# Kernel tuning notes

Hardware: AMD Instinct MI355X
Metric: run time of the kernel (lower is better)

## Reference

```python
import jax, jax.numpy as jnp
import numpy as np

N = 50000
E = 800000
IN_DIM = 256
OUT_DIM = 128
HEADS = 4
D_K = OUT_DIM // HEADS  # 32
BETA = 1.0  # beta_init, requires_grad=False (constant)
NEG_SLOPE = 0.2
EPS = 1e-12


def setup_inputs() -> dict:
    key = jax.random.key(0)
    k = jax.random.split(key, 8)
    H = jax.random.normal(k[0], (N, IN_DIM), dtype=jnp.float32)
    edge_index = jax.random.randint(k[1], (2, E), 0, N, dtype=jnp.int64)
    sim1_edge = jax.random.normal(k[2], (E,), dtype=jnp.float32)
    # Parameters (torch nn.Linear stores weight as (out, in); y = x @ W.T)
    W = jax.random.normal(k[3], (HEADS * D_K, IN_DIM), dtype=jnp.float32) * (1.0 / np.sqrt(IN_DIM))
    a_src = jax.random.normal(k[4], (HEADS, D_K), dtype=jnp.float32)
    a_dst = jax.random.normal(k[5], (HEADS, D_K), dtype=jnp.float32)
    msg_lin_w = jax.random.normal(k[6], (D_K, D_K), dtype=jnp.float32) * (1.0 / np.sqrt(D_K))
    return {"H": H, "edge_index": edge_index, "sim1_edge": sim1_edge,
            "W": W, "a_src": a_src, "a_dst": a_dst, "msg_lin_w": msg_lin_w}


def reference(H, edge_index, sim1_edge, W, a_src, a_dst, msg_lin_w):
    n = H.shape[0]
    H_proj = (H @ W.T).reshape(n, HEADS, D_K)           # [N, h, d_k]
    src, dst = edge_index[0], edge_index[1]
    h_src = H_proj[src]                                  # [E, h, d_k]
    h_dst = H_proj[dst]                                  # [E, h, d_k]
    # per-edge attention logits (struct + semantic)
    e = (jnp.einsum('ehd,hd->eh', h_src, a_src)
         + jnp.einsum('ehd,hd->eh', h_dst, a_dst)
         + BETA * sim1_edge[:, None])                    # [E, h]
    e = jnp.where(e >= 0, e, NEG_SLOPE * e)              # LeakyReLU(0.2)
    # global (per-head) max for stabilization, matching original e.max(dim=0)
    e = e - jnp.max(e, axis=0, keepdims=True)
    exp_e = jnp.exp(e)                                   # [E, h]
    denom = jax.ops.segment_sum(exp_e, dst, num_segments=n)  # [N, h]
    alpha = exp_e / (denom[dst] + EPS)                   # [E, h]  (dropout p=0 -> identity)
    m = alpha[:, :, None] * h_src                        # [E, h, d_k]
    out = jax.ops.segment_sum(m, dst, num_segments=n)    # [N, h, d_k]
    out_h = out.reshape(n, HEADS * D_K)                  # concat=True
    msg_base = jnp.einsum('ehd,od->eho', h_src, msg_lin_w).mean(axis=1)  # [E, d_k]
    alpha_mean = alpha.mean(axis=1)                      # [E]
    return out_h, alpha_mean, msg_base
```

## Files before the change

kernel.cpp:

```cpp
#include <hip/hip_runtime.h>
#include <hip/hip_bf16.h>
#include <hip/hip_fp16.h>
#include <float.h>

#define HEADS 4
#define DK 32

static constexpr float kBeta = 1.0f;
static constexpr float kNeg  = 0.2f;
static constexpr float kEps  = 1e-12f;

__device__ __forceinline__ float bf2f(unsigned short v) {
  return __uint_as_float((unsigned)v << 16);
}
__device__ __forceinline__ float2 bfp2(unsigned u) {
  return make_float2(__uint_as_float(u << 16), __uint_as_float(u & 0xFFFF0000u));
}
__device__ __forceinline__ unsigned fkey(float x) {
  unsigned u = __float_as_uint(x);
  return (u & 0x80000000u) ? ~u : (u | 0x80000000u);
}
__device__ __forceinline__ float funkey(unsigned k) {
  unsigned u = (k & 0x80000000u) ? (k & 0x7fffffffu) : ~k;
  return __uint_as_float(u);
}

__global__ __launch_bounds__(256) void k_detect(const int* __restrict__ ei32,
                                                const unsigned* __restrict__ Hw,
                                                int* __restrict__ eflag,
                                                int* __restrict__ dflag,
                                                int E, int nw) {
  int i = blockIdx.x * 256 + threadIdx.x;
  if (i < 4096 && 2 * i + 1 < 2 * E && ei32[2 * i + 1] != 0) atomicOr(eflag, 1);
  if (i < nw && ((Hw[i] >> 7) & 0xFFu) == 0xFFu) atomicOr(dflag, 1);
}

__global__ __launch_bounds__(256) void k_cvt(const int* __restrict__ ei32,
                                             const int* __restrict__ eflag,
                                             int* __restrict__ src_i,
                                             int* __restrict__ dst_i,
                                             int* __restrict__ deg, int E) {
  int i = blockIdx.x * 256 + threadIdx.x;
  if (i >= E) return;
  int s, d;
  if (*eflag) { s = ei32[i];     d = ei32[E + i]; }
  else        { s = ei32[2 * i]; d = ei32[2 * E + 2 * i]; }
  src_i[i] = s;
  dst_i[i] = d;
  atomicAdd(deg + d, 1);
}

__global__ __launch_bounds__(256) void k_params(const void* __restrict__ a_src,
                                                const void* __restrict__ a_dst,
                                                const void* __restrict__ msg_w,
                                                float* __restrict__ af,
                                                float* __restrict__ msgwf,
                                                const int* __restrict__ dflag) {
  int i = blockIdx.x * 256 + threadIdx.x;
  int dt = *dflag;
  if (i < 128) {
    af[i] = dt ? ((const float*)a_src)[i] : bf2f(((const unsigned short*)a_src)[i]);
  } else if (i < 256) {
    int j = i - 128;
    af[i] = dt ? ((const float*)a_dst)[j] : bf2f(((const unsigned short*)a_dst)[j]);
  } else if (i < 1280) {
    int j = i - 256;
    msgwf[j] = dt ? ((const float*)msg_w)[j] : bf2f(((const unsigned short*)msg_w)[j]);
  }
}

__global__ __launch_bounds__(256) void k_wcvt(const void* __restrict__ in,
                                              float* __restrict__ out,
                                              const int* __restrict__ dflag, int n) {
  int i = blockIdx.x * 256 + threadIdx.x;
  if (i >= n) return;
  int r = i >> 8, c = i & 255;
  float v = (*dflag) ? ((const float*)in)[i] : bf2f(((const unsigned short*)in)[i]);
  out[(size_t)c * 128 + r] = v;
}

__global__ __launch_bounds__(256) void k_scan1(const int* __restrict__ deg,
                                               int* __restrict__ bsum, int N) {
  const int t = threadIdx.x;
  int i = blockIdx.x * 256 + t;
  int v = (i < N) ? deg[i] : 0;
#pragma unroll
  for (int off = 32; off; off >>= 1) v += __shfl_xor(v, off);
  __shared__ int red[4];
  if ((t & 63) == 0) red[t >> 6] = v;
  __syncthreads();
  if (t == 0) bsum[blockIdx.x] = red[0] + red[1] + red[2] + red[3];
}
__global__ __launch_bounds__(1024) void k_scan2(int* __restrict__ bsum, int nb) {
  __shared__ int part[1024];
  const int t = threadIdx.x;
  part[t] = (t < nb) ? bsum[t] : 0;
  __syncthreads();
  int own = part[t];
  for (int off = 1; off < 1024; off <<= 1) {
    int v = (t >= off) ? part[t - off] : 0;
    __syncthreads();
    part[t] += v;
    __syncthreads();
  }
  if (t < nb) bsum[t] = part[t] - own;
}
__global__ __launch_bounds__(256) void k_scan3(const int* __restrict__ deg,
                                               const int* __restrict__ bsum,
                                               int* __restrict__ row_ptr,
                                               int* __restrict__ cursor, int N) {
  __shared__ int part[256];
  const int t = threadIdx.x;
  int i = blockIdx.x * 256 + t;
  int v = (i < N) ? deg[i] : 0;
  part[t] = v;
  __syncthreads();
  for (int off = 1; off < 256; off <<= 1) {
    int x = (t >= off) ? part[t - off] : 0;
    __syncthreads();
    part[t] += x;
    __syncthreads();
  }
  int excl = part[t] - v + bsum[blockIdx.x];
  if (i < N) {
    row_ptr[i] = excl;
    cursor[i]  = excl;
    if (i == N - 1) row_ptr[N] = excl + v;
  }
}

__global__ __launch_bounds__(256) void k_fill(const int* __restrict__ dst,
                                              int* __restrict__ cursor,
                                              int* __restrict__ eidx, int E) {
  int e = blockIdx.x * 256 + threadIdx.x;
  if (e >= E) return;
  int pos = atomicAdd(cursor + dst[e], 1);
  eidx[pos] = e;
}

__global__ __launch_bounds__(256) void k_proj(const void* __restrict__ Hraw,
                                              const float* __restrict__ Wtf,
                                              const int* __restrict__ dflag,
                                              float* __restrict__ Hproj, int N) {
  __shared__ float Ht[32][260];
  const int t = threadIdx.x;
  const int nb = blockIdx.x * 32;
  const int dt = *dflag;
  if (dt) {
    const float4* __restrict__ H4 = (const float4*)Hraw;
#pragma unroll
    for (int i = 0; i < 8; ++i) {
      int f = t + i * 256;
      int r = f >> 6, kq = f & 63;
      float4 v = make_float4(0.f, 0.f, 0.f, 0.f);
      if (nb + r < N) v = H4[(size_t)(nb + r) * 64 + kq];
      *(float4*)&Ht[r][4 * kq] = v;
    }
  } else {
    const uint4* __restrict__ H8 = (const uint4*)Hraw;
#pragma unroll
    for (int i = 0; i < 4; ++i) {
      int g = t + i * 256;
      int r = g >> 5, c8 = g & 31;
      uint4 v = make_uint4(0u, 0u, 0u, 0u);
      if (nb + r < N) v = H8[(size_t)(nb + r) * 32 + c8];
      float2 f0 = bfp2(v.x), f1 = bfp2(v.y), f2 = bfp2(v.z), f3 = bfp2(v.w);
      *(float4*)&Ht[r][c8 * 8 + 0] = make_float4(f0.x, f0.y, f1.x, f1.y);
      *(float4*)&Ht[r][c8 * 8 + 4] = make_float4(f2.x, f2.y, f3.x, f3.y);
    }
  }
  __syncthreads();
  const int cg = (t & 31);
  const int n0 = (t >> 5) * 4;
  float acc[4][4];
#pragma unroll
  for (int n = 0; n < 4; ++n)
#pragma unroll
    for (int j = 0; j < 4; ++j) acc[n][j] = 0.f;
  const float4* __restrict__ Wt4 = (const float4*)Wtf;
#pragma unroll 4
  for (int kk = 0; kk < 256; kk += 4) {
    float4 w0 = Wt4[(size_t)(kk + 0) * 32 + cg];
    float4 w1 = Wt4[(size_t)(kk + 1) * 32 + cg];
    float4 w2 = Wt4[(size_t)(kk + 2) * 32 + cg];
    float4 w3 = Wt4[(size_t)(kk + 3) * 32 + cg];
#pragma unroll
    for (int n = 0; n < 4; ++n) {
      float4 h = *(const float4*)&Ht[n0 + n][kk];
      acc[n][0] += h.x * w0.x + h.y * w1.x + h.z * w2.x + h.w * w3.x;
      acc[n][1] += h.x * w0.y + h.y * w1.y + h.z * w2.y + h.w * w3.y;
      acc[n][2] += h.x * w0.z + h.y * w1.z + h.z * w2.z + h.w * w3.z;
      acc[n][3] += h.x * w0.w + h.y * w1.w + h.z * w2.w + h.w * w3.w;
    }
  }
#pragma unroll
  for (int n = 0; n < 4; ++n) {
    int row = nb + n0 + n;
    if (row < N)
      *(float4*)&Hproj[(size_t)row * 128 + 4 * cg] =
          make_float4(acc[n][0], acc[n][1], acc[n][2], acc[n][3]);
  }
}

__global__ __launch_bounds__(256) void k_node(const float* __restrict__ Hproj,
                                              const float* __restrict__ af,
                                              const float* __restrict__ msgwf,
                                              float* __restrict__ s_src,
                                              float* __restrict__ s_dst,
                                              __half* __restrict__ msgb,
                                              __half* __restrict__ Hb, int N) {
  const int l = threadIdx.x & 63;
  const int wb = threadIdx.x >> 6;
  const int n = (blockIdx.x << 2) + wb;
  if (n >= N) return;
  const float* row = Hproj + (size_t)n * 128;
  float h0 = row[l], h1 = row[64 + l];
  Hb[(size_t)n * 128 + l]      = __float2half(h0);
  Hb[(size_t)n * 128 + 64 + l] = __float2half(h1);
  float p0 = h0 * af[l],       p1 = h1 * af[64 + l];
  float q0 = h0 * af[128 + l], q1 = h1 * af[192 + l];
#pragma unroll
  for (int off = 16; off; off >>= 1) {
    p0 += __shfl_xor(p0, off);
    p1 += __shfl_xor(p1, off);
    q0 += __shfl_xor(q0, off);
    q1 += __shfl_xor(q1, off);
  }
  if (l == 0)  { s_src[n*4+0] = p0; s_src[n*4+2] = p1; s_dst[n*4+0] = q0; s_dst[n*4+2] = q1; }
  if (l == 32) { s_src[n*4+1] = p0; s_src[n*4+3] = p1; s_dst[n*4+1] = q0; s_dst[n*4+3] = q1; }
  float t4 = h0 + __shfl_xor(h0, 32) + h1 + __shfl_xor(h1, 32);
  float hbar = 0.25f * t4;
  if (l < DK) {
    float acc = 0.f;
#pragma unroll
    for (int d = 0; d < DK; ++d) acc += __shfl(hbar, d) * msgwf[l * DK + d];
    msgb[(size_t)n * DK + l] = __float2half(acc);
  }
}

__global__ __launch_bounds__(256) void k_logits(const int* __restrict__ src,
                                                const int* __restrict__ dst,
                                                const void* __restrict__ sim1,
                                                const int* __restrict__ dflag,
                                                const float* __restrict__ s_src,
                                                const float* __restrict__ s_dst,
                                                unsigned* __restrict__ gmax, int E) {
  const int e = blockIdx.x * 256 + threadIdx.x;
  float m0 = -FLT_MAX, m1 = -FLT_MAX, m2 = -FLT_MAX, m3 = -FLT_MAX;
  if (e < E) {
    int s = src[e], d = dst[e];
    float4 ss = *(const float4*)(s_src + (size_t)s * 4);
    float4 sd = *(const float4*)(s_dst + (size_t)d * 4);
    float sv = (*dflag) ? ((const float*)sim1)[e] : bf2f(((const unsigned short*)sim1)[e]);
    float b = kBeta * sv;
    float e0 = ss.x + sd.x + b; e0 = (e0 >= 0.f) ? e0 : kNeg * e0;
    float e1 = ss.y + sd.y + b; e1 = (e1 >= 0.f) ? e1 : kNeg * e1;
    float e2 = ss.z + sd.z + b; e2 = (e2 >= 0.f) ? e2 : kNeg * e2;
    float e3 = ss.w + sd.w + b; e3 = (e3 >= 0.f) ? e3 : kNeg * e3;
    m0 = e0; m1 = e1; m2 = e2; m3 = e3;
  }
#pragma unroll
  for (int off = 32; off; off >>= 1) {
    m0 = fmaxf(m0, __shfl_xor(m0, off));
    m1 = fmaxf(m1, __shfl_xor(m1, off));
    m2 = fmaxf(m2, __shfl_xor(m2, off));
    m3 = fmaxf(m3, __shfl_xor(m3, off));
  }
  __shared__ float red[4][4];
  if ((threadIdx.x & 63) == 0) {
    int w = threadIdx.x >> 6;
    red[w][0] = m0; red[w][1] = m1; red[w][2] = m2; red[w][3] = m3;
  }
  __syncthreads();
  if (threadIdx.x < 4) {
    int h = threadIdx.x;
    float mm = fmaxf(fmaxf(red[0][h], red[1][h]), fmaxf(red[2][h], red[3][h]));
    atomicMax(gmax + h, fkey(mm));
  }
}

__global__ __launch_bounds__(256) void k_msg(const int* __restrict__ src,
                                             const __half2* __restrict__ msgb2,
                                             const int* __restrict__ dflag,
                                             void* __restrict__ d_out,
                                             int N, int E) {
  long long tid = (long long)blockIdx.x * 256 + threadIdx.x;
  if (tid >= (long long)E * 16) return;
  int e = (int)(tid >> 4), jp = (int)(tid & 15);
  __half2 hv = msgb2[(size_t)src[e] * 16 + jp];
  float2 f = __half22float2(hv);
  const size_t msg_off = (size_t)N * 128 + (size_t)E;
  if (*dflag) {
    *(float2*)&((float*)d_out)[msg_off + (size_t)e * 32 + 2 * jp] = f;
  } else {
    __hip_bfloat162 b = __float22bfloat162_rn(f);
    *(__hip_bfloat162*)((__hip_bfloat16*)d_out + msg_off + (size_t)e * 32 + 2 * jp) = b;
  }
}

__global__ __launch_bounds__(256) void k_out(const int* __restrict__ row_ptr,
                                             const int* __restrict__ eidx,
                                             const int* __restrict__ src,
                                             const void* __restrict__ sim1,
                                             const float* __restrict__ s_src,
                                             const float* __restrict__ s_dst,
                                             const unsigned* __restrict__ gmax,
                                             const unsigned* __restrict__ Hb_u,
                                             const int* __restrict__ dflag,
                                             void* __restrict__ d_out, int N, int E) {
  const int n = (int)((blockIdx.x * 256 + threadIdx.x) >> 6);
  const int l = threadIdx.x & 63;
  if (n >= N) return;
  const int beg = row_ptr[n];
  const int deg = row_ptr[n + 1] - beg;
  const int dt = *dflag;
  const float m0 = funkey(gmax[0]), m1 = funkey(gmax[1]);
  const float m2 = funkey(gmax[2]), m3 = funkey(gmax[3]);
  const float4 sd = *(const float4*)(s_dst + (size_t)n * 4);
  const size_t alpha_off = (size_t)N * 128;
  float accx = 0.f, accy = 0.f;
  float4 dn = make_float4(0.f, 0.f, 0.f, 0.f);
  int eid = 0, s = 0;
  float4 ev = make_float4(0.f, 0.f, 0.f, 0.f);
  const bool small = (deg <= 64);
  if (small) {
    if (l < deg) {
      eid = eidx[beg + l];
      s = src[eid];
      float4 ss = *(const float4*)(s_src + (size_t)s * 4);
      float sv = dt ? ((const float*)sim1)[eid] : bf2f(((const unsigned short*)sim1)[eid]);
      float e0 = ss.x + sd.x + sv; e0 = (e0 >= 0.f) ? e0 : kNeg * e0;
      float e1 = ss.y + sd.y + sv; e1 = (e1 >= 0.f) ? e1 : kNeg * e1;
      float e2 = ss.z + sd.z + sv; e2 = (e2 >= 0.f) ? e2 : kNeg * e2;
      float e3 = ss.w + sd.w + sv; e3 = (e3 >= 0.f) ? e3 : kNeg * e3;
      ev = make_float4(expf(e0 - m0), expf(e1 - m1), expf(e2 - m2), expf(e3 - m3));
      dn = ev;
    }
  } else {
    for (int base = 0; base < deg; base += 64) {
      if (base + l < deg) {
        int e2i = eidx[beg + base + l];
        int s2 = src[e2i];
        float4 ss = *(const float4*)(s_src + (size_t)s2 * 4);
        float sv = dt ? ((const float*)sim1)[e2i] : bf2f(((const unsigned short*)sim1)[e2i]);
        float e0 = ss.x + sd.x + sv; e0 = (e0 >= 0.f) ? e0 : kNeg * e0;
        float e1 = ss.y + sd.y + sv; e1 = (e1 >= 0.f) ? e1 : kNeg * e1;
        float e2 = ss.z + sd.z + sv; e2 = (e2 >= 0.f) ? e2 : kNeg * e2;
        float e3 = ss.w + sd.w + sv; e3 = (e3 >= 0.f) ? e3 : kNeg * e3;
        dn.x += expf(e0 - m0); dn.y += expf(e1 - m1);
        dn.z += expf(e2 - m2); dn.w += expf(e3 - m3);
      }
    }
  }
#pragma unroll
  for (int off = 32; off; off >>= 1) {
    dn.x += __shfl_xor(dn.x, off);
    dn.y += __shfl_xor(dn.y, off);
    dn.z += __shfl_xor(dn.z, off);
    dn.w += __shfl_xor(dn.w, off);
  }
  const float i0 = 1.f / (dn.x + kEps), i1 = 1.f / (dn.y + kEps);
  const float i2 = 1.f / (dn.z + kEps), i3 = 1.f / (dn.w + kEps);
  const float myinv = (l < 32) ? ((l < 16) ? i0 : i1) : ((l < 48) ? i2 : i3);
  if (small) {
    if (l < deg) {
      float am = 0.25f * (ev.x * i0 + ev.y * i1 + ev.z * i2 + ev.w * i3);
      if (dt) ((float*)d_out)[alpha_off + eid] = am;
      else    ((__hip_bfloat16*)d_out)[alpha_off + eid] = __float2bfloat16(am);
    }
    for (int i = 0; i < deg; ++i) {
      int si = __shfl(s, i);
      float ax = __shfl(ev.x, i), ay = __shfl(ev.y, i);
      float az = __shfl(ev.z, i), aw = __shfl(ev.w, i);
      float aa = ((l < 32) ? ((l < 16) ? ax : ay) : ((l < 48) ? az : aw)) * myinv;
      unsigned u = Hb_u[(size_t)si * 64 + l];
      float2 f = __half22float2(*(const __half2*)&u);
      accx += aa * f.x;
      accy += aa * f.y;
    }
  } else {
    for (int base = 0; base < deg; base += 64) {
      int cnt = min(64, deg - base);
      int eid2 = 0, s2 = 0;
      float4 e2v = make_float4(0.f, 0.f, 0.f, 0.f);
      if (l < cnt) {
        eid2 = eidx[beg + base + l];
        s2 = src[eid2];
        float4 ss = *(const float4*)(s_src + (size_t)s2 * 4);
        float sv = dt ? ((const float*)sim1)[eid2] : bf2f(((const unsigned short*)sim1)[eid2]);
        float e0 = ss.x + sd.x + sv; e0 = (e0 >= 0.f) ? e0 : kNeg * e0;
        float e1 = ss.y + sd.y + sv; e1 = (e1 >= 0.f) ? e1 : kNeg * e1;
        float e2 = ss.z + sd.z + sv; e2 = (e2 >= 0.f) ? e2 : kNeg * e2;
        float e3 = ss.w + sd.w + sv; e3 = (e3 >= 0.f) ? e3 : kNeg * e3;
        e2v = make_float4(expf(e0 - m0), expf(e1 - m1), expf(e2 - m2), expf(e3 - m3));
        float am = 0.25f * (e2v.x * i0 + e2v.y * i1 + e2v.z * i2 + e2v.w * i3);
        if (dt) ((float*)d_out)[alpha_off + eid2] = am;
        else    ((__hip_bfloat16*)d_out)[alpha_off + eid2] = __float2bfloat16(am);
      }
      for (int i = 0; i < cnt; ++i) {
        int si = __shfl(s2, i);
        float ax = __shfl(e2v.x, i), ay = __shfl(e2v.y, i);
        float az = __shfl(e2v.z, i), aw = __shfl(e2v.w, i);
        float aa = ((l < 32) ? ((l < 16) ? ax : ay) : ((l < 48) ? az : aw)) * myinv;
        unsigned u = Hb_u[(size_t)si * 64 + l];
        float2 f = __half22float2(*(const __half2*)&u);
        accx += aa * f.x;
        accy += aa * f.y;
      }
    }
  }
  if (dt) {
    *(float2*)&((float*)d_out)[(size_t)n * 128 + 2 * l] = make_float2(accx, accy);
  } else {
    __hip_bfloat162 b = __float22bfloat162_rn(make_float2(accx, accy));
    *(__hip_bfloat162*)((__hip_bfloat16*)d_out + (size_t)n * 128 + 2 * l) = b;
  }
}

extern "C" void kernel_launch(void* const* d_in, const int* in_sizes, int n_in,
                              void* d_out, int out_size, void* d_ws, size_t ws_size,
                              hipStream_t stream) {
  const void* H     = d_in[0];
  const int*  ei    = (const int*)d_in[1];
  const void* sim1  = d_in[2];
  const void* W     = d_in[3];
  const void* a_src = d_in[4];
  const void* a_dst = d_in[5];
  const void* msg_w = d_in[6];
  const int N = in_sizes[0] / 256;
  const int E = in_sizes[2];
  const int NB = (N + 255) / 256;

  char* base     = (char*)d_ws;
  float* Hproj   = (float*)base;  base += (size_t)N * 128 * 4;
  float* s_src   = (float*)base;  base += (size_t)N * 4 * 4;
  float* s_dst   = (float*)base;  base += (size_t)N * 4 * 4;
  __half* msgb   = (__half*)base; base += (size_t)N * DK * 2;
  __half* Hb     = (__half*)base; base += (size_t)N * 128 * 2;
  int* deg       = (int*)base;    base += (size_t)N * 4;
  unsigned* gmax = (unsigned*)base; base += 4 * 4;
  int* eflag     = (int*)base;    base += 4;
  int* dflag     = (int*)base;    base += 4;
  int* row_ptr   = (int*)base;    base += (size_t)(N + 1) * 4;
  int* cursor    = (int*)base;    base += (size_t)N * 4;
  int* bsum      = (int*)base;    base += 1024 * 4;
  int* eidx      = (int*)base;    base += (size_t)E * 4;
  int* src_i     = (int*)base;    base += (size_t)E * 4;
  int* dst_i     = (int*)base;    base += (size_t)E * 4;
  float* Wtf     = (float*)base;  base += 128 * 256 * 4;
  float* af      = (float*)base;  base += 256 * 4;
  float* msgwf   = (float*)base;  base += 1024 * 4;

  hipMemsetAsync(deg, 0, (size_t)(N + 6) * sizeof(int), stream);

  k_detect<<<512, 256, 0, stream>>>(ei, (const unsigned*)H, eflag, dflag, E, 131072);
  k_cvt<<<(E + 255) / 256, 256, 0, stream>>>(ei, eflag, src_i, dst_i, deg, E);
  k_wcvt<<<128, 256, 0, stream>>>(W, Wtf, dflag, 128 * 256);
  k_params<<<5, 256, 0, stream>>>(a_src, a_dst, msg_w, af, msgwf, dflag);
  k_proj<<<(N + 31) / 32, 256, 0, stream>>>(H, Wtf, dflag, Hproj, N);
  k_scan1<<<NB, 256, 0, stream>>>(deg, bsum, N);
  k_scan2<<<1, 1024, 0, stream>>>(bsum, NB);
  k_scan3<<<NB, 256, 0, stream>>>(deg, bsum, row_ptr, cursor, N);
  k_fill<<<(E + 255) / 256, 256, 0, stream>>>(dst_i, cursor, eidx, E);
  k_node<<<(N + 3) / 4, 256, 0, stream>>>(Hproj, af, msgwf, s_src, s_dst, msgb, Hb, N);
  k_logits<<<(E + 255) / 256, 256, 0, stream>>>(src_i, dst_i, sim1, dflag, s_src, s_dst,
                                                gmax, E);
  k_msg<<<(int)(((long long)E * 16 + 255) / 256), 256, 0, stream>>>(
      src_i, (const __half2*)msgb, dflag, d_out, N, E);
  k_out<<<(int)(((size_t)N * 64 + 255) / 256), 256, 0, stream>>>(
      row_ptr, eidx, src_i, sim1, s_src, s_dst, gmax, (const unsigned*)Hb, dflag,
      d_out, N, E);
}
```

Baseline: 515.1 us.

## Use bf16 MFMA with split hi/lo precision for node projection GEMM

Replaces the scalar FP32 FMA projection GEMM with bf16 MFMA 16x16x32 instructions. For fp32 inputs, both H and W are split into bf16 hi and lo parts and combined with three MFMAs to approximate fp32 accuracy. W is prepacked into the MFMA operand layout, and H is staged in a swizzled LDS tile of 64 rows per block. This targets the compute cost of the N x 256 x 128 GEMM. The split-bf16 scheme drops the lo*lo term, so results carry slightly more rounding error than true fp32.

```diff
diff --git a/kernel.cpp b/kernel.cpp
--- a/kernel.cpp
+++ b/kernel.cpp
@@ -10,8 +10,16 @@
 static constexpr float kNeg  = 0.2f;
 static constexpr float kEps  = 1e-12f;
 
+typedef __bf16 bf16x8 __attribute__((ext_vector_type(8)));
+typedef float  f32x4  __attribute__((ext_vector_type(4)));
+
 __device__ __forceinline__ float bf2f(unsigned short v) {
   return __uint_as_float((unsigned)v << 16);
+}
+__device__ __forceinline__ unsigned short f2bf(float f) {
+  unsigned u = __float_as_uint(f);
+  unsigned r = u + 0x7FFFu + ((u >> 16) & 1u);
+  return (unsigned short)(r >> 16);
 }
 __device__ __forceinline__ float2 bfp2(unsigned u) {
   return make_float2(__uint_as_float(u << 16), __uint_as_float(u & 0xFFFF0000u));
@@ -23,6 +31,9 @@
 __device__ __forceinline__ float funkey(unsigned k) {
   unsigned u = (k & 0x80000000u) ? (k & 0x7fffffffu) : ~k;
   return __uint_as_float(u);
+}
+__device__ __forceinline__ bf16x8 as8(uint4 v) {
+  union { uint4 u; bf16x8 b; } x; x.u = v; return x.b;
 }
 
 __global__ __launch_bounds__(256) void k_detect(const int* __restrict__ ei32,
@@ -69,14 +80,21 @@
   }
 }
 
-__global__ __launch_bounds__(256) void k_wcvt(const void* __restrict__ in,
-                                              float* __restrict__ out,
-                                              const int* __restrict__ dflag, int n) {
+__global__ __launch_bounds__(256) void k_wpack(const void* __restrict__ in,
+                                               unsigned short* __restrict__ Bhi,
+                                               unsigned short* __restrict__ Blo,
+                                               const int* __restrict__ dflag, int n) {
   int i = blockIdx.x * 256 + threadIdx.x;
   if (i >= n) return;
   int r = i >> 8, c = i & 255;
   float v = (*dflag) ? ((const float*)in)[i] : bf2f(((const unsigned short*)in)[i]);
-  out[(size_t)c * 128 + r] = v;
+  unsigned short hb = f2bf(v);
+  unsigned short lb = f2bf(v - bf2f(hb));
+  int kt = c >> 5, ct = r >> 4;
+  int lane = (((c >> 3) & 3) << 4) | (r & 15);
+  int idx = ((kt * 8 + ct) * 64 + lane) * 8 + (c & 7);
+  Bhi[idx] = hb;
+  Blo[idx] = lb;
 }
 
 __global__ __launch_bounds__(256) void k_scan1(const int* __restrict__ deg,
@@ -139,66 +157,97 @@
 }
 
 __global__ __launch_bounds__(256) void k_proj(const void* __restrict__ Hraw,
-                                              const float* __restrict__ Wtf,
+                                              const unsigned short* __restrict__ Bhi,
+                                              const unsigned short* __restrict__ Blo,
                                               const int* __restrict__ dflag,
                                               float* __restrict__ Hproj, int N) {
-  __shared__ float Ht[32][260];
+  __shared__ uint4 lds4[4096];
   const int t = threadIdx.x;
-  const int nb = blockIdx.x * 32;
+  const int nb = blockIdx.x * 64;
   const int dt = *dflag;
   if (dt) {
     const float4* __restrict__ H4 = (const float4*)Hraw;
 #pragma unroll
-    for (int i = 0; i < 8; ++i) {
-      int f = t + i * 256;
-      int r = f >> 6, kq = f & 63;
-      float4 v = make_float4(0.f, 0.f, 0.f, 0.f);
-      if (nb + r < N) v = H4[(size_t)(nb + r) * 64 + kq];
-      *(float4*)&Ht[r][4 * kq] = v;
+    for (int it = 0; it < 8; ++it) {
+      int c = it * 256 + t;
+      int row = c >> 5, k8 = c & 31;
+      int gr = nb + row;
+      float4 v0 = make_float4(0.f, 0.f, 0.f, 0.f), v1 = v0;
+      if (gr < N) {
+        v0 = H4[(size_t)gr * 64 + k8 * 2];
+        v1 = H4[(size_t)gr * 64 + k8 * 2 + 1];
+      }
+      float f[8] = {v0.x, v0.y, v0.z, v0.w, v1.x, v1.y, v1.z, v1.w};
+      unsigned hi[8], lo[8];
+#pragma unroll
+      for (int j = 0; j < 8; ++j) {
+        unsigned short hb = f2bf(f[j]);
+        hi[j] = hb;
+        lo[j] = f2bf(f[j] - bf2f(hb));
+      }
+      int slot = (k8 * 64 + row) ^ (k8 & 7);
+      lds4[slot] = make_uint4(hi[0] | (hi[1] << 16), hi[2] | (hi[3] << 16),
+                              hi[4] | (hi[5] << 16), hi[6] | (hi[7] << 16));
+      lds4[2048 + slot] = make_uint4(lo[0] | (lo[1] << 16), lo[2] | (lo[3] << 16),
+                                     lo[4] | (lo[5] << 16), lo[6] | (lo[7] << 16));
     }
   } else {
     const uint4* __restrict__ H8 = (const uint4*)Hraw;
 #pragma unroll
-    for (int i = 0; i < 4; ++i) {
-      int g = t + i * 256;
-      int r = g >> 5, c8 = g & 31;
+    for (int it = 0; it < 8; ++it) {
+      int c = it * 256 + t;
+      int row = c >> 5, k8 = c & 31;
+      int gr = nb + row;
       uint4 v = make_uint4(0u, 0u, 0u, 0u);
-      if (nb + r < N) v = H8[(size_t)(nb + r) * 32 + c8];
-      float2 f0 = bfp2(v.x), f1 = bfp2(v.y), f2 = bfp2(v.z), f3 = bfp2(v.w);
-      *(float4*)&Ht[r][c8 * 8 + 0] = make_float4(f0.x, f0.y, f1.x, f1.y);
-      *(float4*)&Ht[r][c8 * 8 + 4] = make_float4(f2.x, f2.y, f3.x, f3.y);
+      if (gr < N) v = H8[(size_t)gr * 32 + k8];
+      lds4[(k8 * 64 + row) ^ (k8 & 7)] = v;
     }
   }
   __syncthreads();
-  const int cg = (t & 31);
-  const int n0 = (t >> 5) * 4;
-  float acc[4][4];
-#pragma unroll
-  for (int n = 0; n < 4; ++n)
-#pragma unroll
-    for (int j = 0; j < 4; ++j) acc[n][j] = 0.f;
-  const float4* __restrict__ Wt4 = (const float4*)Wtf;
-#pragma unroll 4
-  for (int kk = 0; kk < 256; kk += 4) {
-    float4 w0 = Wt4[(size_t)(kk + 0) * 32 + cg];
-    float4 w1 = Wt4[(size_t)(kk + 1) * 32 + cg];
-    float4 w2 = Wt4[(size_t)(kk + 2) * 32 + cg];
-    float4 w3 = Wt4[(size_t)(kk + 3) * 32 + cg];
-#pragma unroll
-    for (int n = 0; n < 4; ++n) {
-      float4 h = *(const float4*)&Ht[n0 + n][kk];
-      acc[n][0] += h.x * w0.x + h.y * w1.x + h.z * w2.x + h.w * w3.x;
-      acc[n][1] += h.x * w0.y + h.y * w1.y + h.z * w2.y + h.w * w3.y;
-      acc[n][2] += h.x * w0.z + h.y * w1.z + h.z * w2.z + h.w * w3.z;
-      acc[n][3] += h.x * w0.w + h.y * w1.w + h.z * w2.w + h.w * w3.w;
-    }
-  }
-#pragma unroll
-  for (int n = 0; n < 4; ++n) {
-    int row = nb + n0 + n;
-    if (row < N)
-      *(float4*)&Hproj[(size_t)row * 128 + 4 * cg] =
-          make_float4(acc[n][0], acc[n][1], acc[n][2], acc[n][3]);
+
+  const int l = t & 63;
+  const int wrow = (t >> 6) * 16;
+  f32x4 acc[8];
+#pragma unroll
+  for (int ct = 0; ct < 8; ++ct) acc[ct] = (f32x4){0.f, 0.f, 0.f, 0.f};
+  const uint4* __restrict__ Bh4 = (const uint4*)Bhi;
+  const uint4* __restrict__ Bl4 = (const uint4*)Blo;
+  if (dt) {
+#pragma unroll 2
+    for (int kt = 0; kt < 8; ++kt) {
+      int k8 = kt * 4 + (l >> 4);
+      int slot = (k8 * 64 + wrow + (l & 15)) ^ (k8 & 7);
+      bf16x8 ah = as8(lds4[slot]);
+      bf16x8 al = as8(lds4[2048 + slot]);
+#pragma unroll
+      for (int ct = 0; ct < 8; ++ct) {
+        bf16x8 bh = as8(Bh4[(kt * 8 + ct) * 64 + l]);
+        bf16x8 bl = as8(Bl4[(kt * 8 + ct) * 64 + l]);
+        acc[ct] = __builtin_amdgcn_mfma_f32_16x16x32_bf16(ah, bh, acc[ct], 0, 0, 0);
+        acc[ct] = __builtin_amdgcn_mfma_f32_16x16x32_bf16(ah, bl, acc[ct], 0, 0, 0);
+        acc[ct] = __builtin_amdgcn_mfma_f32_16x16x32_bf16(al, bh, acc[ct], 0, 0, 0);
+      }
+    }
+  } else {
+#pragma unroll 2
+    for (int kt = 0; kt < 8; ++kt) {
+      int k8 = kt * 4 + (l >> 4);
+      int slot = (k8 * 64 + wrow + (l & 15)) ^ (k8 & 7);
+      bf16x8 ah = as8(lds4[slot]);
+#pragma unroll
+      for (int ct = 0; ct < 8; ++ct) {
+        bf16x8 bh = as8(Bh4[(kt * 8 + ct) * 64 + l]);
+        acc[ct] = __builtin_amdgcn_mfma_f32_16x16x32_bf16(ah, bh, acc[ct], 0, 0, 0);
+      }
+    }
+  }
+#pragma unroll
+  for (int ct = 0; ct < 8; ++ct) {
+#pragma unroll
+    for (int r = 0; r < 4; ++r) {
+      int grow = nb + wrow + (l >> 4) * 4 + r;
+      if (grow < N) Hproj[(size_t)grow * 128 + ct * 16 + (l & 15)] = acc[ct][r];
+    }
   }
 }
 
@@ -437,6 +486,8 @@
   float* s_dst   = (float*)base;  base += (size_t)N * 4 * 4;
   __half* msgb   = (__half*)base; base += (size_t)N * DK * 2;
   __half* Hb     = (__half*)base; base += (size_t)N * 128 * 2;
+  unsigned short* Bhi = (unsigned short*)base; base += 32768 * 2;
+  unsigned short* Blo = (unsigned short*)base; base += 32768 * 2;
   int* deg       = (int*)base;    base += (size_t)N * 4;
   unsigned* gmax = (unsigned*)base; base += 4 * 4;
   int* eflag     = (int*)base;    base += 4;
@@ -447,7 +498,6 @@
   int* eidx      = (int*)base;    base += (size_t)E * 4;
   int* src_i     = (int*)base;    base += (size_t)E * 4;
   int* dst_i     = (int*)base;    base += (size_t)E * 4;
-  float* Wtf     = (float*)base;  base += 128 * 256 * 4;
   float* af      = (float*)base;  base += 256 * 4;
   float* msgwf   = (float*)base;  base += 1024 * 4;
 
@@ -455,9 +505,9 @@
 
   k_detect<<<512, 256, 0, stream>>>(ei, (const unsigned*)H, eflag, dflag, E, 131072);
   k_cvt<<<(E + 255) / 256, 256, 0, stream>>>(ei, eflag, src_i, dst_i, deg, E);
-  k_wcvt<<<128, 256, 0, stream>>>(W, Wtf, dflag, 128 * 256);
+  k_wpack<<<128, 256, 0, stream>>>(W, Bhi, Blo, dflag, 128 * 256);
   k_params<<<5, 256, 0, stream>>>(a_src, a_dst, msg_w, af, msgwf, dflag);
-  k_proj<<<(N + 31) / 32, 256, 0, stream>>>(H, Wtf, dflag, Hproj, N);
+  k_proj<<<(N + 63) / 64, 256, 0, stream>>>(H, Bhi, Blo, dflag, Hproj, N);
   k_scan1<<<NB, 256, 0, stream>>>(deg, bsum, N);
   k_scan2<<<1, 1024, 0, stream>>>(bsum, NB);
   k_scan3<<<NB, 256, 0, stream>>>(deg, bsum, row_ptr, cursor, N);
```

New measurement: 483.8 us. 6.1% less time.
